# Optimization experiments

Measured on AMD Instinct MI355X. Metric: run time of the kernel, lower is better.

## Reference

```python
import jax, jax.numpy as jnp
import numpy as np

D_MODEL = 1024
NUM_HEADS = 16
HEAD_DIM = D_MODEL // NUM_HEADS
B, S = 4, 2048


def setup_inputs() -> dict:
    key = jax.random.key(0)
    ks = jax.random.split(key, 11)
    sc = 1.0 / np.sqrt(D_MODEL)
    return {
        "query": jax.random.normal(ks[0], (B, S, D_MODEL), jnp.float32),
        "key": jax.random.normal(ks[1], (B, S, D_MODEL), jnp.float32),
        "value": jax.random.normal(ks[2], (B, S, D_MODEL), jnp.float32),
        "Wq": jax.random.normal(ks[3], (D_MODEL, D_MODEL), jnp.float32) * sc,
        "bq": jnp.zeros((D_MODEL,), jnp.float32),
        "Wk": jax.random.normal(ks[4], (D_MODEL, D_MODEL), jnp.float32) * sc,
        "bk": jnp.zeros((D_MODEL,), jnp.float32),
        "Wv": jax.random.normal(ks[5], (D_MODEL, D_MODEL), jnp.float32) * sc,
        "bv": jnp.zeros((D_MODEL,), jnp.float32),
        "Wo": jax.random.normal(ks[6], (D_MODEL, D_MODEL), jnp.float32) * sc,
        "bo": jnp.zeros((D_MODEL,), jnp.float32),
    }


def _split_heads(x):
    b, s, _ = x.shape
    return x.reshape(b, s, NUM_HEADS, HEAD_DIM).transpose(0, 2, 1, 3)  # [B,H,S,Dh]


def reference(query, key, value, Wq, bq, Wk, bk, Wv, bv, Wo, bo):
    q = _split_heads(query @ Wq + bq)
    k = _split_heads(key @ Wk + bk)
    v = _split_heads(value @ Wv + bv)
    scores = jnp.einsum("bhqd,bhkd->bhqk", q, k) / np.sqrt(HEAD_DIM)
    attn = jax.nn.softmax(scores, axis=-1)
    out = jnp.einsum("bhqk,bhkd->bhqd", attn, v)
    out = out.transpose(0, 2, 1, 3).reshape(query.shape[0], -1, D_MODEL)
    return out @ Wo + bo
```

## Files before the change

kernel.cpp:

```cpp
#include <hip/hip_runtime.h>

typedef unsigned short u16;
typedef unsigned int   u32;
typedef unsigned long long u64;
typedef __attribute__((ext_vector_type(8))) short bf16x8;
typedef __attribute__((ext_vector_type(4))) float f32x4;

#define S_  2048
#define DH  64
#define DM  1024
#define BS  8192
#define CS  0.18033688011112042f

static __device__ __forceinline__ float bf2f(u16 v){ return __uint_as_float(((u32)v)<<16); }
static __device__ __forceinline__ u16 f2bf(float f){
  u32 x = __float_as_uint(f);
  return (u16)((x + 0x7fffu + ((x>>16)&1u)) >> 16);
}
#if __has_builtin(__builtin_amdgcn_cvt_pk_bf16_f32)
static __device__ __forceinline__ u32 pk2(float x, float y){
  typedef __attribute__((ext_vector_type(2))) __bf16 bf2v;
  union { bf2v v; u32 u; } c; c.v = __builtin_amdgcn_cvt_pk_bf16_f32(x, y); return c.u;
}
#else
static __device__ __forceinline__ u32 pk2(float x, float y){
  return (u32)f2bf(x) | ((u32)f2bf(y) << 16);
}
#endif
#if __has_builtin(__builtin_amdgcn_exp2f)
#define EXP2F(x) __builtin_amdgcn_exp2f(x)
#else
#define EXP2F(x) exp2f(x)
#endif

static __device__ __forceinline__ void dma16(const u16* g, const u16* l){
  __builtin_amdgcn_global_load_lds(
      (const __attribute__((address_space(1))) u32*)(u64)(uintptr_t)g,
      (__attribute__((address_space(3))) u32*)(u32)(u64)(uintptr_t)l, 16, 0, 0);
}

static __device__ __forceinline__ bf16x8 lds_frag(const u16* p){
  union { bf16x8 f; uint2 u[2]; } w;
  w.u[0] = *(const uint2*)(p);
  w.u[1] = *(const uint2*)(p+4);
  return w.f;
}
static __device__ __forceinline__ bf16x8 frag16v(const u16* p){
  union { bf16x8 f; uint4 u; } w;
  w.u = *(const uint4*)p;
  return w.f;
}
static __device__ __forceinline__ void stage16_bf(const u16* __restrict__ g, u16* s){
  uint4 a = *(const uint4*)g;
  uint4 b = *(const uint4*)(g+8);
  *(uint2*)(s+0)  = make_uint2(a.x,a.y);
  *(uint2*)(s+4)  = make_uint2(a.z,a.w);
  *(uint2*)(s+8)  = make_uint2(b.x,b.y);
  *(uint2*)(s+12) = make_uint2(b.z,b.w);
}
static __device__ __forceinline__ void stage16_f32(const float* __restrict__ g, u16* s){
  float4 a0 = ((const float4*)g)[0];
  float4 a1 = ((const float4*)g)[1];
  float4 a2 = ((const float4*)g)[2];
  float4 a3 = ((const float4*)g)[3];
  *(uint2*)(s+0)  = make_uint2(pk2(a0.x,a0.y), pk2(a0.z,a0.w));
  *(uint2*)(s+4)  = make_uint2(pk2(a1.x,a1.y), pk2(a1.z,a1.w));
  *(uint2*)(s+8)  = make_uint2(pk2(a2.x,a2.y), pk2(a2.z,a2.w));
  *(uint2*)(s+12) = make_uint2(pk2(a3.x,a3.y), pk2(a3.z,a3.w));
}

__global__ __launch_bounds__(256) void prep(
    const void* __restrict__ w0, const void* __restrict__ w1,
    const void* __restrict__ w2, const void* __restrict__ w3,
    u16* t0, u16* t1, u16* t2, u16* t3,
    const void* __restrict__ a0, const void* __restrict__ a1,
    const void* __restrict__ a2,
    u16* c0, u16* c1, u16* c2, const int f32f){
  __shared__ u16 tile[32][33];
  int z = blockIdx.z;
  int tid = threadIdx.x;
  bool f32 = f32f != 0;
  if (z < 4){
    const void* in = z==0?w0 : z==1?w1 : z==2?w2 : w3;
    u16* out = z==0?t0 : z==1?t1 : z==2?t2 : t3;
    int tx = tid & 31, ty = tid >> 5;
    int c  = blockIdx.x*32 + tx;
    int r0 = blockIdx.y*32;
    for (int i=ty;i<32;i+=8){
      long off = (long)(r0+i)*DM + c;
      tile[i][tx] = f32 ? f2bf(((const float*)in)[off]) : ((const u16*)in)[off];
    }
    __syncthreads();
    int rr = r0 + tx, cb = blockIdx.x*32;
    for (int i=ty;i<32;i+=8) out[(long)(cb+i)*DM + rr] = tile[tx][i];
  } else {
    if (!f32) return;
    const void* in = z==4?a0 : z==5?a1 : a2;
    u16* out = z==4?c0 : z==5?c1 : c2;
    long lb = (long)blockIdx.y*32 + blockIdx.x;
    long base = (lb*256 + tid)*8;
    #pragma unroll
    for (int it=0; it<4; it++){
      long i = base + (long)it*2097152;
      const float4* p = (const float4*)((const float*)in + i);
      float4 x = p[0], y = p[1];
      *(uint4*)(out + i) = make_uint4(pk2(x.x,x.y), pk2(x.z,x.w), pk2(y.x,y.y), pk2(y.z,y.w));
    }
  }
}

template<int ADMA>
__global__ __launch_bounds__(256) void gemm_qkv(
    const void* __restrict__ A0, const void* __restrict__ A1, const void* __restrict__ A2,
    const u16* __restrict__ W0, const u16* __restrict__ W1, const u16* __restrict__ W2,
    const void* __restrict__ bv0, const void* __restrict__ bv1, const void* __restrict__ bv2,
    u16* C0, u16* C1, u16* C2, const int f32f){
  constexpr int AST = ADMA ? 32 : 36;
  constexpr int NB  = ADMA ? 2 : 1;
  __shared__ __align__(16) u16 As[NB][128*AST];
  __shared__ __align__(16) u16 Bs[NB][128*32];
  int z = blockIdx.z;
  const void* A  = z==0?A0 : z==1?A1 : A2;
  const u16* BT  = z==0?W0 : z==1?W1 : W2;
  const void* bias = z==0?bv0 : z==1?bv1 : bv2;
  u16* C = z==0?C0 : z==1?C1 : C2;
  const bool aF32 = (!ADMA) && (f32f != 0);
  const bool bF32 = (f32f != 0);
  int tid = threadIdx.x;
  int by = blockIdx.x, bx = blockIdx.y;
  int lane = tid & 63, w = tid >> 6;
  int t = lane & 15, q = lane >> 4;
  int wr = w >> 1, wc = w & 1;
  f32x4 acc[4][4];
  #pragma unroll
  for(int i=0;i<4;i++) for(int j=0;j<4;j++) for(int k=0;k<4;k++) acc[i][j][k]=0.f;

  if constexpr (ADMA){
    int sl = (lane & 7) ^ (lane >> 3);
    int srow = ((lane >> 3) << 1) + (sl >> 2);
    const u16* gA = (const u16*)A + ((long)(by*128 + w*32 + srow)*DM + (sl&3)*8);
    const u16* gB = BT            + ((long)(bx*128 + w*32 + srow)*DM + (sl&3)*8);
    const int lb = w*1024;
    int rdo = ((t>>1)<<6) + (((((t&1)<<2) | q) ^ (t>>1)) << 3);
    dma16(gA,         &As[0][lb]);
    dma16(gA + 16*DM, &As[0][lb + 512]);
    dma16(gB,         &Bs[0][lb]);
    dma16(gB + 16*DM, &Bs[0][lb + 512]);
    for (int k0=0; k0<DM; k0+=32){
      int cur = (k0>>5)&1;
      if (k0+32 < DM){
        dma16(gA + k0+32,         &As[cur^1][lb]);
        dma16(gA + k0+32 + 16*DM, &As[cur^1][lb + 512]);
        dma16(gB + k0+32,         &Bs[cur^1][lb]);
        dma16(gB + k0+32 + 16*DM, &Bs[cur^1][lb + 512]);
        asm volatile("s_waitcnt vmcnt(4)" ::: "memory");
      } else {
        asm volatile("s_waitcnt vmcnt(0)" ::: "memory");
      }
      __builtin_amdgcn_s_barrier();
      bf16x8 af[4], bfr[4];
      const u16* Ar = &As[cur][wr*2048 + rdo];
      const u16* Br = &Bs[cur][wc*2048 + rdo];
      #pragma unroll
      for (int rt=0;rt<4;rt++) af[rt]  = frag16v(Ar + rt*512);
      #pragma unroll
      for (int ct=0;ct<4;ct++) bfr[ct] = frag16v(Br + ct*512);
      #pragma unroll
      for (int rt=0;rt<4;rt++)
        #pragma unroll
        for (int ct=0;ct<4;ct++)
          acc[rt][ct] = __builtin_amdgcn_mfma_f32_16x16x32_bf16(af[rt], bfr[ct], acc[rt][ct], 0,0,0);
      __builtin_amdgcn_s_barrier();
    }
  } else {
    const u16* gB = BT + ((long)(bx*128 + w*32 + (lane>>2))*DM + (lane&3)*8);
    long aoff = (long)(by*128 + (tid>>1))*DM + (tid&1)*16;
    const u16* ArdB = &As[0][(wr*64 + t)*AST + q*8];
    const u16* BrdB = &Bs[0][(wc*64 + t)*32  + q*8];
    for (int k0=0; k0<DM; k0+=32){
      dma16(gB + k0,         &Bs[0][w*1024]);
      dma16(gB + 16*DM + k0, &Bs[0][w*1024 + 512]);
      u16* AsW = &As[0][(tid>>1)*36 + (tid&1)*16];
      if (aF32) stage16_f32((const float*)A + aoff + k0, AsW);
      else      stage16_bf ((const u16*)A  + aoff + k0, AsW);
      __syncthreads();
      bf16x8 af[4], bfr[4];
      #pragma unroll
      for (int rt=0;rt<4;rt++) af[rt]  = lds_frag(ArdB + rt*16*AST);
      #pragma unroll
      for (int ct=0;ct<4;ct++) bfr[ct] = lds_frag(BrdB + ct*16*32);
      #pragma unroll
      for (int rt=0;rt<4;rt++)
        #pragma unroll
        for (int ct=0;ct<4;ct++)
          acc[rt][ct] = __builtin_amdgcn_mfma_f32_16x16x32_bf16(af[rt], bfr[ct], acc[rt][ct], 0,0,0);
      __syncthreads();
    }
  }

  float scale = (z==0) ? CS : 1.0f;
  #pragma unroll
  for (int ct=0;ct<4;ct++){
    int col = bx*128 + wc*64 + ct*16 + t;
    float bvv = bF32 ? ((const float*)bias)[col] : bf2f(((const u16*)bias)[col]);
    #pragma unroll
    for (int rt=0;rt<4;rt++){
      int row0 = by*128 + wr*64 + rt*16 + q*4;
      if (z == 2){
        int bb = row0 >> 11, s = row0 & 2047;
        long vbase = (long)bb*2097152 + (long)col*2048
                   + (s & ~63) + ((rt>>1)<<5) + (q<<3) + ((rt&1)<<2);
        u32 lo = pk2(acc[rt][ct][0]+bvv, acc[rt][ct][1]+bvv);
        u32 hi = pk2(acc[rt][ct][2]+bvv, acc[rt][ct][3]+bvv);
        *(uint2*)(C + vbase) = make_uint2(lo,hi);
      } else {
        #pragma unroll
        for (int r=0;r<4;r++)
          C[(long)(row0+r)*DM + col] = f2bf((acc[rt][ct][r] + bvv)*scale);
      }
    }
  }
}

__global__ __launch_bounds__(256) void gemm_o(const u16* __restrict__ A,
    const u16* __restrict__ BT, const void* __restrict__ bias, void* __restrict__ C,
    const int f32f){
  __shared__ __align__(16) u16 As[2][128*32];
  __shared__ __align__(16) u16 Bs[2][128*32];
  const int f = f32f;
  int tid = threadIdx.x;
  int by = blockIdx.x, bx = blockIdx.y;
  int lane = tid & 63, w = tid >> 6;
  int t = lane & 15, q = lane >> 4;
  int wr = w >> 1, wc = w & 1;
  f32x4 acc[4][4];
  #pragma unroll
  for(int i=0;i<4;i++) for(int j=0;j<4;j++) for(int k=0;k<4;k++) acc[i][j][k]=0.f;

  int sl = (lane & 7) ^ (lane >> 3);
  int srow = ((lane >> 3) << 1) + (sl >> 2);
  const u16* gA = A  + ((long)(by*128 + w*32 + srow)*DM + (sl&3)*8);
  const u16* gB = BT + ((long)(bx*128 + w*32 + srow)*DM + (sl&3)*8);
  const int lb = w*1024;
  int rdo = ((t>>1)<<6) + (((((t&1)<<2) | q) ^ (t>>1)) << 3);
  dma16(gA,         &As[0][lb]);
  dma16(gA + 16*DM, &As[0][lb + 512]);
  dma16(gB,         &Bs[0][lb]);
  dma16(gB + 16*DM, &Bs[0][lb + 512]);
  for (int k0=0; k0<DM; k0+=32){
    int cur = (k0>>5)&1;
    if (k0+32 < DM){
      dma16(gA + k0+32,         &As[cur^1][lb]);
      dma16(gA + k0+32 + 16*DM, &As[cur^1][lb + 512]);
      dma16(gB + k0+32,         &Bs[cur^1][lb]);
      dma16(gB + k0+32 + 16*DM, &Bs[cur^1][lb + 512]);
      asm volatile("s_waitcnt vmcnt(4)" ::: "memory");
    } else {
      asm volatile("s_waitcnt vmcnt(0)" ::: "memory");
    }
    __builtin_amdgcn_s_barrier();
    bf16x8 af[4], bfr[4];
    const u16* Ar = &As[cur][wr*2048 + rdo];
    const u16* Br = &Bs[cur][wc*2048 + rdo];
    #pragma unroll
    for (int rt=0;rt<4;rt++) af[rt]  = frag16v(Ar + rt*512);
    #pragma unroll
    for (int ct=0;ct<4;ct++) bfr[ct] = frag16v(Br + ct*512);
    #pragma unroll
    for (int rt=0;rt<4;rt++)
      #pragma unroll
      for (int ct=0;ct<4;ct++)
        acc[rt][ct] = __builtin_amdgcn_mfma_f32_16x16x32_bf16(af[rt], bfr[ct], acc[rt][ct], 0,0,0);
    __builtin_amdgcn_s_barrier();
  }
  #pragma unroll
  for (int ct=0;ct<4;ct++){
    int col = bx*128 + wc*64 + ct*16 + t;
    float bvv = f ? ((const float*)bias)[col] : bf2f(((const u16*)bias)[col]);
    #pragma unroll
    for (int rt=0;rt<4;rt++){
      int row0 = by*128 + wr*64 + rt*16 + q*4;
      #pragma unroll
      for (int r=0;r<4;r++){
        long idx = (long)(row0+r)*DM + col;
        float v = acc[rt][ct][r] + bvv;
        if (f) ((float*)C)[idx] = v;
        else   ((u16*)C)[idx]  = f2bf(v);
      }
    }
  }
}

__global__ __launch_bounds__(256,4) void attn5(const u16* __restrict__ Q,
    const u16* __restrict__ Kb, const u16* __restrict__ Vt, u16* __restrict__ O){
  __shared__ __align__(16) u16 Ks[2][4096];
  __shared__ __align__(16) u16 Vs[2][4096];
  int tid = threadIdx.x;
  int bid = blockIdx.x;
  int qt = bid >> 6;
  int s6 = bid & 63;
  int bh = (s6 & 7)*8 + (s6 >> 3);
  int b = bh >> 4, h = bh & 15;
  int lane = tid & 63, w = tid >> 6;
  int t = lane & 15, q = lane >> 4;

  const u16* Qbase = Q + ((long)(b*S_ + qt*128 + w*32 + t)*DM + h*DH + q*8);
  bf16x8 qf[2][2];
  qf[0][0] = frag16v(Qbase);
  qf[0][1] = frag16v(Qbase + 32);
  qf[1][0] = frag16v(Qbase + 16*DM);
  qf[1][1] = frag16v(Qbase + 16*DM + 32);

  int r0 = tid >> 3;
  int cb = ((tid & 7) * 16) ^ ((r0 & 7) << 4);
  const char* gK = (const char*)Kb + (((long)(b*S_ + r0)*DM + h*DH) << 1) + cb;
  const char* gV = (const char*)Vt + ((((long)bh << 17) + ((long)r0 << 11)) << 1) + cb;
  const long gK1 = ((long)32*DM) << 1;
  const long gV1 = ((long)32*S_) << 1;
  const int ld0 = w*512, ld1 = 2048 + w*512;

  f32x4 o[2][4];
  #pragma unroll
  for (int i=0;i<2;i++) for (int j=0;j<4;j++) for (int k=0;k<4;k++) o[i][j][k]=0.f;
  f32x4 o4[2];
  #pragma unroll
  for (int i=0;i<2;i++) for (int k=0;k<4;k++) o4[i][k]=0.f;

  const f32x4 z4 = {0.f, 0.f, 0.f, 0.f};

  union { bf16x8 f; u32 u[4]; } vone;
  { u32 ovv = (t==0) ? 0x3F803F80u : 0u;
    vone.u[0]=ovv; vone.u[1]=ovv; vone.u[2]=ovv; vone.u[3]=ovv; }

  const int xorv = (t & 7) << 4;

  dma16((const u16*)(gK),       &Ks[0][ld0]);
  dma16((const u16*)(gK + gK1), &Ks[0][ld1]);
  dma16((const u16*)(gV),       &Vs[0][ld0]);
  dma16((const u16*)(gV + gV1), &Vs[0][ld1]);

  for (int kt=0; kt<32; kt++){
    int cur = kt & 1;
    if (kt < 31){
      long ko = ((long)(kt+1)*64*DM) << 1;
      long vo = (long)(kt+1) << 7;
      dma16((const u16*)(gK + ko),       &Ks[cur^1][ld0]);
      dma16((const u16*)(gK + ko + gK1), &Ks[cur^1][ld1]);
      dma16((const u16*)(gV + vo),       &Vs[cur^1][ld0]);
      dma16((const u16*)(gV + vo + gV1), &Vs[cur^1][ld1]);
      asm volatile("s_waitcnt vmcnt(4)" ::: "memory");
    } else {
      asm volatile("s_waitcnt vmcnt(0)" ::: "memory");
    }
    __builtin_amdgcn_s_barrier();

    const u16* Kc = Ks[cur];
    const u16* Vc = Vs[cur];

    f32x4 sacc[2][4];
    {
      int off = ((q*16) ^ xorv) >> 1;
      bf16x8 k0 = frag16v(Kc + (t     )*64 + off);
      bf16x8 k1 = frag16v(Kc + (16 + t)*64 + off);
      bf16x8 k2 = frag16v(Kc + (32 + t)*64 + off);
      bf16x8 k3 = frag16v(Kc + (48 + t)*64 + off);
      __builtin_amdgcn_s_setprio(1);
      #pragma unroll
      for (int rt=0; rt<2; rt++){
        sacc[rt][0] = __builtin_amdgcn_mfma_f32_16x16x32_bf16(k0, qf[rt][0], z4, 0,0,0);
        sacc[rt][1] = __builtin_amdgcn_mfma_f32_16x16x32_bf16(k1, qf[rt][0], z4, 0,0,0);
        sacc[rt][2] = __builtin_amdgcn_mfma_f32_16x16x32_bf16(k2, qf[rt][0], z4, 0,0,0);
        sacc[rt][3] = __builtin_amdgcn_mfma_f32_16x16x32_bf16(k3, qf[rt][0], z4, 0,0,0);
      }
      __builtin_amdgcn_s_setprio(0);
    }
    {
      int off = ((64 + q*16) ^ xorv) >> 1;
      bf16x8 k0 = frag16v(Kc + (t     )*64 + off);
      bf16x8 k1 = frag16v(Kc + (16 + t)*64 + off);
      bf16x8 k2 = frag16v(Kc + (32 + t)*64 + off);
      bf16x8 k3 = frag16v(Kc + (48 + t)*64 + off);
      __builtin_amdgcn_s_setprio(1);
      #pragma unroll
      for (int rt=0; rt<2; rt++){
        sacc[rt][0] = __builtin_amdgcn_mfma_f32_16x16x32_bf16(k0, qf[rt][1], sacc[rt][0],0,0,0);
        sacc[rt][1] = __builtin_amdgcn_mfma_f32_16x16x32_bf16(k1, qf[rt][1], sacc[rt][1],0,0,0);
        sacc[rt][2] = __builtin_amdgcn_mfma_f32_16x16x32_bf16(k2, qf[rt][1], sacc[rt][2],0,0,0);
        sacc[rt][3] = __builtin_amdgcn_mfma_f32_16x16x32_bf16(k3, qf[rt][1], sacc[rt][3],0,0,0);
      }
      __builtin_amdgcn_s_setprio(0);
    }

    union { bf16x8 f; u32 u[4]; } af[2][2];
    #pragma unroll
    for (int rt=0; rt<2; rt++){
      float ev[4][4];
      #pragma unroll
      for (int c=0; c<4; c++)
        #pragma unroll
        for (int r=0; r<4; r++) ev[c][r] = EXP2F(sacc[rt][c][r]);
      #pragma unroll
      for (int ks=0; ks<2; ks++){
        af[rt][ks].u[0] = pk2(ev[2*ks  ][0], ev[2*ks  ][1]);
        af[rt][ks].u[1] = pk2(ev[2*ks  ][2], ev[2*ks  ][3]);
        af[rt][ks].u[2] = pk2(ev[2*ks+1][0], ev[2*ks+1][1]);
        af[rt][ks].u[3] = pk2(ev[2*ks+1][2], ev[2*ks+1][3]);
      }
    }

    #pragma unroll
    for (int ks=0; ks<2; ks++){
      int off = ((ks*64 + q*16) ^ xorv) >> 1;
      bf16x8 v0 = frag16v(Vc + (t     )*64 + off);
      bf16x8 v1 = frag16v(Vc + (16 + t)*64 + off);
      bf16x8 v2 = frag16v(Vc + (32 + t)*64 + off);
      bf16x8 v3 = frag16v(Vc + (48 + t)*64 + off);
      __builtin_amdgcn_s_setprio(1);
      #pragma unroll
      for (int rt=0; rt<2; rt++){
        o[rt][0] = __builtin_amdgcn_mfma_f32_16x16x32_bf16(af[rt][ks].f, v0, o[rt][0],0,0,0);
        o[rt][1] = __builtin_amdgcn_mfma_f32_16x16x32_bf16(af[rt][ks].f, v1, o[rt][1],0,0,0);
        o[rt][2] = __builtin_amdgcn_mfma_f32_16x16x32_bf16(af[rt][ks].f, v2, o[rt][2],0,0,0);
        o[rt][3] = __builtin_amdgcn_mfma_f32_16x16x32_bf16(af[rt][ks].f, v3, o[rt][3],0,0,0);
        o4[rt]   = __builtin_amdgcn_mfma_f32_16x16x32_bf16(af[rt][ks].f, vone.f, o4[rt],0,0,0);
      }
      __builtin_amdgcn_s_setprio(0);
    }
    __builtin_amdgcn_s_barrier();
  }

  #pragma unroll
  for (int rt=0; rt<2; rt++){
    #pragma unroll
    for (int r=0; r<4; r++){
      float l = __shfl(o4[rt][r], lane & 48);
      float inv = 1.f / l;
      int row = qt*128 + w*32 + rt*16 + q*4 + r;
      #pragma unroll
      for (int ct=0; ct<4; ct++)
        O[(long)(b*S_ + row)*DM + h*DH + ct*16 + t] = f2bf(o[rt][ct][r] * inv);
    }
  }
}

extern "C" void kernel_launch(void* const* d_in, const int* in_sizes, int n_in,
                              void* d_out, int out_size, void* d_ws, size_t ws_size,
                              hipStream_t stream){
  (void)n_in; (void)out_size;
  const void* xq = d_in[0];
  const void* xk = d_in[1];
  const void* xv = d_in[2];
  const void* Wq = d_in[3];
  const void* bq = d_in[4];
  const void* Wk = d_in[5];
  const void* bk = d_in[6];
  const void* Wv = d_in[7];
  const void* bv = d_in[8];
  const void* Wo = d_in[9];
  const void* bo = d_in[10];

  const long NT = (long)BS*DM;
  int f32f = 1;
  if (in_sizes && in_sizes[0] == (int)(NT*2)) f32f = 0;

  u16* base = (u16*)((char*)d_ws + 256);
  u16* Qb  = base;
  u16* Kbf = base + NT;
  u16* Vt  = base + 2*NT;
  u16* WqT = base + 3*NT;
  u16* WkT = WqT + (long)DM*DM;
  u16* WvT = WkT + (long)DM*DM;
  u16* WoT = WvT + (long)DM*DM;
  u16* Xc0 = WoT + (long)DM*DM;
  u16* Xc1 = Xc0 + NT;
  u16* Xc2 = Xc1 + NT;
  size_t need_pre = 256 + (size_t)(6*NT + 4*(long)DM*DM)*2;
  bool pre = ws_size >= need_pre;

  dim3 gb(256,1,1);
  int nz = (pre && f32f) ? 7 : 4;
  prep<<<dim3(32,32,nz), gb, 0, stream>>>(Wq, Wk, Wv, Wo,
      WqT, WkT, WvT, WoT, xq, xk, xv, Xc0, Xc1, Xc2, f32f);

  if (pre){
    const void* Aq = f32f ? (const void*)Xc0 : xq;
    const void* Ak = f32f ? (const void*)Xc1 : xk;
    const void* Av = f32f ? (const void*)Xc2 : xv;
    gemm_qkv<1><<<dim3(64,8,3), gb, 0, stream>>>(Aq, Ak, Av,
        WqT, WkT, WvT, bq, bk, bv, Qb, Kbf, Vt, f32f);
  } else {
    gemm_qkv<0><<<dim3(64,8,3), gb, 0, stream>>>(xq, xk, xv,
        WqT, WkT, WvT, bq, bk, bv, Qb, Kbf, Vt, f32f);
  }

  attn5<<<dim3(1024,1,1), gb, 0, stream>>>(Qb, Kbf, Vt, Qb );

  gemm_o<<<dim3(64,8,1), gb, 0, stream>>>(Qb, WoT, bo, d_out, f32f);
}
```

Baseline: 350.7 us.

## Enlarge GEMM tiles to 256x128x64 with 512 threads and XOR-swizzled LDS

```diff
diff --git a/kernel.cpp b/kernel.cpp
--- a/kernel.cpp
+++ b/kernel.cpp
@@ -39,34 +39,10 @@
       (__attribute__((address_space(3))) u32*)(u32)(u64)(uintptr_t)l, 16, 0, 0);
 }
 
-static __device__ __forceinline__ bf16x8 lds_frag(const u16* p){
-  union { bf16x8 f; uint2 u[2]; } w;
-  w.u[0] = *(const uint2*)(p);
-  w.u[1] = *(const uint2*)(p+4);
-  return w.f;
-}
 static __device__ __forceinline__ bf16x8 frag16v(const u16* p){
   union { bf16x8 f; uint4 u; } w;
   w.u = *(const uint4*)p;
   return w.f;
-}
-static __device__ __forceinline__ void stage16_bf(const u16* __restrict__ g, u16* s){
-  uint4 a = *(const uint4*)g;
-  uint4 b = *(const uint4*)(g+8);
-  *(uint2*)(s+0)  = make_uint2(a.x,a.y);
-  *(uint2*)(s+4)  = make_uint2(a.z,a.w);
-  *(uint2*)(s+8)  = make_uint2(b.x,b.y);
-  *(uint2*)(s+12) = make_uint2(b.z,b.w);
-}
-static __device__ __forceinline__ void stage16_f32(const float* __restrict__ g, u16* s){
-  float4 a0 = ((const float4*)g)[0];
-  float4 a1 = ((const float4*)g)[1];
-  float4 a2 = ((const float4*)g)[2];
-  float4 a3 = ((const float4*)g)[3];
-  *(uint2*)(s+0)  = make_uint2(pk2(a0.x,a0.y), pk2(a0.z,a0.w));
-  *(uint2*)(s+4)  = make_uint2(pk2(a1.x,a1.y), pk2(a1.z,a1.w));
-  *(uint2*)(s+8)  = make_uint2(pk2(a2.x,a2.y), pk2(a2.z,a2.w));
-  *(uint2*)(s+12) = make_uint2(pk2(a3.x,a3.y), pk2(a3.z,a3.w));
 }
 
 __global__ __launch_bounds__(256) void prep(
@@ -109,22 +85,19 @@
   }
 }
 
-template<int ADMA>
-__global__ __launch_bounds__(256) void gemm_qkv(
-    const void* __restrict__ A0, const void* __restrict__ A1, const void* __restrict__ A2,
+
+__global__ __launch_bounds__(512) void gemm_qkv(
+    const u16* __restrict__ A0, const u16* __restrict__ A1, const u16* __restrict__ A2,
     const u16* __restrict__ W0, const u16* __restrict__ W1, const u16* __restrict__ W2,
     const void* __restrict__ bv0, const void* __restrict__ bv1, const void* __restrict__ bv2,
     u16* C0, u16* C1, u16* C2, const int f32f){
-  constexpr int AST = ADMA ? 32 : 36;
-  constexpr int NB  = ADMA ? 2 : 1;
-  __shared__ __align__(16) u16 As[NB][128*AST];
-  __shared__ __align__(16) u16 Bs[NB][128*32];
+  __shared__ __align__(16) u16 As[2][256*64];
+  __shared__ __align__(16) u16 Bs[2][128*64];
   int z = blockIdx.z;
-  const void* A  = z==0?A0 : z==1?A1 : A2;
-  const u16* BT  = z==0?W0 : z==1?W1 : W2;
+  const u16* A  = z==0?A0 : z==1?A1 : A2;
+  const u16* BT = z==0?W0 : z==1?W1 : W2;
   const void* bias = z==0?bv0 : z==1?bv1 : bv2;
   u16* C = z==0?C0 : z==1?C1 : C2;
-  const bool aF32 = (!ADMA) && (f32f != 0);
   const bool bF32 = (f32f != 0);
   int tid = threadIdx.x;
   int by = blockIdx.x, bx = blockIdx.y;
@@ -135,66 +108,47 @@
   #pragma unroll
   for(int i=0;i<4;i++) for(int j=0;j<4;j++) for(int k=0;k<4;k++) acc[i][j][k]=0.f;
 
-  if constexpr (ADMA){
-    int sl = (lane & 7) ^ (lane >> 3);
-    int srow = ((lane >> 3) << 1) + (sl >> 2);
-    const u16* gA = (const u16*)A + ((long)(by*128 + w*32 + srow)*DM + (sl&3)*8);
-    const u16* gB = BT            + ((long)(bx*128 + w*32 + srow)*DM + (sl&3)*8);
-    const int lb = w*1024;
-    int rdo = ((t>>1)<<6) + (((((t&1)<<2) | q) ^ (t>>1)) << 3);
-    dma16(gA,         &As[0][lb]);
-    dma16(gA + 16*DM, &As[0][lb + 512]);
-    dma16(gB,         &Bs[0][lb]);
-    dma16(gB + 16*DM, &Bs[0][lb + 512]);
-    for (int k0=0; k0<DM; k0+=32){
-      int cur = (k0>>5)&1;
-      if (k0+32 < DM){
-        dma16(gA + k0+32,         &As[cur^1][lb]);
-        dma16(gA + k0+32 + 16*DM, &As[cur^1][lb + 512]);
-        dma16(gB + k0+32,         &Bs[cur^1][lb]);
-        dma16(gB + k0+32 + 16*DM, &Bs[cur^1][lb + 512]);
-        asm volatile("s_waitcnt vmcnt(4)" ::: "memory");
-      } else {
-        asm volatile("s_waitcnt vmcnt(0)" ::: "memory");
-      }
-      __builtin_amdgcn_s_barrier();
+  int sl = (lane & 7) ^ (lane >> 3);
+  const u16* gA = A  + ((long)(by*256 + w*8 + (lane>>3))*DM + sl*8);
+  const u16* gB = BT + ((long)(bx*128 + w*8 + (lane>>3))*DM + sl*8);
+
+  #pragma unroll
+  for (int i=0;i<4;i++) dma16(gA + (long)i*64*DM,      &As[0][(i*64 + w*8)*64]);
+  #pragma unroll
+  for (int j=0;j<2;j++) dma16(gB + (long)j*64*DM,      &Bs[0][(j*64 + w*8)*64]);
+  #pragma unroll
+  for (int i=0;i<4;i++) dma16(gA + (long)i*64*DM + 64, &As[1][(i*64 + w*8)*64]);
+  #pragma unroll
+  for (int j=0;j<2;j++) dma16(gB + (long)j*64*DM + 64, &Bs[1][(j*64 + w*8)*64]);
+
+  for (int kt=0; kt<16; kt++){
+    int buf = kt & 1;
+    if (kt < 15) asm volatile("s_waitcnt vmcnt(6)" ::: "memory");
+    else         asm volatile("s_waitcnt vmcnt(0)" ::: "memory");
+    __builtin_amdgcn_s_barrier();
+    #pragma unroll
+    for (int kk=0; kk<2; kk++){
       bf16x8 af[4], bfr[4];
-      const u16* Ar = &As[cur][wr*2048 + rdo];
-      const u16* Br = &Bs[cur][wc*2048 + rdo];
-      #pragma unroll
-      for (int rt=0;rt<4;rt++) af[rt]  = frag16v(Ar + rt*512);
-      #pragma unroll
-      for (int ct=0;ct<4;ct++) bfr[ct] = frag16v(Br + ct*512);
+      int so = (((kk*4 + q) ^ (t&7)) << 3);
+      #pragma unroll
+      for (int rt=0;rt<4;rt++) af[rt]  = frag16v(&As[buf][(wr*64 + rt*16 + t)*64 + so]);
+      #pragma unroll
+      for (int ct=0;ct<4;ct++) bfr[ct] = frag16v(&Bs[buf][(wc*64 + ct*16 + t)*64 + so]);
+      __builtin_amdgcn_s_setprio(1);
       #pragma unroll
       for (int rt=0;rt<4;rt++)
         #pragma unroll
         for (int ct=0;ct<4;ct++)
           acc[rt][ct] = __builtin_amdgcn_mfma_f32_16x16x32_bf16(af[rt], bfr[ct], acc[rt][ct], 0,0,0);
-      __builtin_amdgcn_s_barrier();
-    }
-  } else {
-    const u16* gB = BT + ((long)(bx*128 + w*32 + (lane>>2))*DM + (lane&3)*8);
-    long aoff = (long)(by*128 + (tid>>1))*DM + (tid&1)*16;
-    const u16* ArdB = &As[0][(wr*64 + t)*AST + q*8];
-    const u16* BrdB = &Bs[0][(wc*64 + t)*32  + q*8];
-    for (int k0=0; k0<DM; k0+=32){
-      dma16(gB + k0,         &Bs[0][w*1024]);
-      dma16(gB + 16*DM + k0, &Bs[0][w*1024 + 512]);
-      u16* AsW = &As[0][(tid>>1)*36 + (tid&1)*16];
-      if (aF32) stage16_f32((const float*)A + aoff + k0, AsW);
-      else      stage16_bf ((const u16*)A  + aoff + k0, AsW);
-      __syncthreads();
-      bf16x8 af[4], bfr[4];
-      #pragma unroll
-      for (int rt=0;rt<4;rt++) af[rt]  = lds_frag(ArdB + rt*16*AST);
-      #pragma unroll
-      for (int ct=0;ct<4;ct++) bfr[ct] = lds_frag(BrdB + ct*16*32);
-      #pragma unroll
-      for (int rt=0;rt<4;rt++)
-        #pragma unroll
-        for (int ct=0;ct<4;ct++)
-          acc[rt][ct] = __builtin_amdgcn_mfma_f32_16x16x32_bf16(af[rt], bfr[ct], acc[rt][ct], 0,0,0);
-      __syncthreads();
+      __builtin_amdgcn_s_setprio(0);
+    }
+    __builtin_amdgcn_s_barrier();
+    if (kt + 2 < 16){
+      int k0 = (kt+2)*64;
+      #pragma unroll
+      for (int i=0;i<4;i++) dma16(gA + (long)i*64*DM + k0, &As[buf][(i*64 + w*8)*64]);
+      #pragma unroll
+      for (int j=0;j<2;j++) dma16(gB + (long)j*64*DM + k0, &Bs[buf][(j*64 + w*8)*64]);
     }
   }
 
@@ -205,7 +159,7 @@
     float bvv = bF32 ? ((const float*)bias)[col] : bf2f(((const u16*)bias)[col]);
     #pragma unroll
     for (int rt=0;rt<4;rt++){
-      int row0 = by*128 + wr*64 + rt*16 + q*4;
+      int row0 = by*256 + wr*64 + rt*16 + q*4;
       if (z == 2){
         int bb = row0 >> 11, s = row0 & 2047;
         long vbase = (long)bb*2097152 + (long)col*2048
@@ -222,11 +176,11 @@
   }
 }
 
-__global__ __launch_bounds__(256) void gemm_o(const u16* __restrict__ A,
+__global__ __launch_bounds__(512) void gemm_o(const u16* __restrict__ A,
     const u16* __restrict__ BT, const void* __restrict__ bias, void* __restrict__ C,
     const int f32f){
-  __shared__ __align__(16) u16 As[2][128*32];
-  __shared__ __align__(16) u16 Bs[2][128*32];
+  __shared__ __align__(16) u16 As[2][256*64];
+  __shared__ __align__(16) u16 Bs[2][128*64];
   const int f = f32f;
   int tid = threadIdx.x;
   int by = blockIdx.x, bx = blockIdx.y;
@@ -238,48 +192,56 @@
   for(int i=0;i<4;i++) for(int j=0;j<4;j++) for(int k=0;k<4;k++) acc[i][j][k]=0.f;
 
   int sl = (lane & 7) ^ (lane >> 3);
-  int srow = ((lane >> 3) << 1) + (sl >> 2);
-  const u16* gA = A  + ((long)(by*128 + w*32 + srow)*DM + (sl&3)*8);
-  const u16* gB = BT + ((long)(bx*128 + w*32 + srow)*DM + (sl&3)*8);
-  const int lb = w*1024;
-  int rdo = ((t>>1)<<6) + (((((t&1)<<2) | q) ^ (t>>1)) << 3);
-  dma16(gA,         &As[0][lb]);
-  dma16(gA + 16*DM, &As[0][lb + 512]);
-  dma16(gB,         &Bs[0][lb]);
-  dma16(gB + 16*DM, &Bs[0][lb + 512]);
-  for (int k0=0; k0<DM; k0+=32){
-    int cur = (k0>>5)&1;
-    if (k0+32 < DM){
-      dma16(gA + k0+32,         &As[cur^1][lb]);
-      dma16(gA + k0+32 + 16*DM, &As[cur^1][lb + 512]);
-      dma16(gB + k0+32,         &Bs[cur^1][lb]);
-      dma16(gB + k0+32 + 16*DM, &Bs[cur^1][lb + 512]);
-      asm volatile("s_waitcnt vmcnt(4)" ::: "memory");
-    } else {
-      asm volatile("s_waitcnt vmcnt(0)" ::: "memory");
-    }
-    __builtin_amdgcn_s_barrier();
-    bf16x8 af[4], bfr[4];
-    const u16* Ar = &As[cur][wr*2048 + rdo];
-    const u16* Br = &Bs[cur][wc*2048 + rdo];
-    #pragma unroll
-    for (int rt=0;rt<4;rt++) af[rt]  = frag16v(Ar + rt*512);
-    #pragma unroll
-    for (int ct=0;ct<4;ct++) bfr[ct] = frag16v(Br + ct*512);
-    #pragma unroll
-    for (int rt=0;rt<4;rt++)
-      #pragma unroll
-      for (int ct=0;ct<4;ct++)
-        acc[rt][ct] = __builtin_amdgcn_mfma_f32_16x16x32_bf16(af[rt], bfr[ct], acc[rt][ct], 0,0,0);
-    __builtin_amdgcn_s_barrier();
-  }
+  const u16* gA = A  + ((long)(by*256 + w*8 + (lane>>3))*DM + sl*8);
+  const u16* gB = BT + ((long)(bx*128 + w*8 + (lane>>3))*DM + sl*8);
+
+  #pragma unroll
+  for (int i=0;i<4;i++) dma16(gA + (long)i*64*DM,      &As[0][(i*64 + w*8)*64]);
+  #pragma unroll
+  for (int j=0;j<2;j++) dma16(gB + (long)j*64*DM,      &Bs[0][(j*64 + w*8)*64]);
+  #pragma unroll
+  for (int i=0;i<4;i++) dma16(gA + (long)i*64*DM + 64, &As[1][(i*64 + w*8)*64]);
+  #pragma unroll
+  for (int j=0;j<2;j++) dma16(gB + (long)j*64*DM + 64, &Bs[1][(j*64 + w*8)*64]);
+
+  for (int kt=0; kt<16; kt++){
+    int buf = kt & 1;
+    if (kt < 15) asm volatile("s_waitcnt vmcnt(6)" ::: "memory");
+    else         asm volatile("s_waitcnt vmcnt(0)" ::: "memory");
+    __builtin_amdgcn_s_barrier();
+    #pragma unroll
+    for (int kk=0; kk<2; kk++){
+      bf16x8 af[4], bfr[4];
+      int so = (((kk*4 + q) ^ (t&7)) << 3);
+      #pragma unroll
+      for (int rt=0;rt<4;rt++) af[rt]  = frag16v(&As[buf][(wr*64 + rt*16 + t)*64 + so]);
+      #pragma unroll
+      for (int ct=0;ct<4;ct++) bfr[ct] = frag16v(&Bs[buf][(wc*64 + ct*16 + t)*64 + so]);
+      __builtin_amdgcn_s_setprio(1);
+      #pragma unroll
+      for (int rt=0;rt<4;rt++)
+        #pragma unroll
+        for (int ct=0;ct<4;ct++)
+          acc[rt][ct] = __builtin_amdgcn_mfma_f32_16x16x32_bf16(af[rt], bfr[ct], acc[rt][ct], 0,0,0);
+      __builtin_amdgcn_s_setprio(0);
+    }
+    __builtin_amdgcn_s_barrier();
+    if (kt + 2 < 16){
+      int k0 = (kt+2)*64;
+      #pragma unroll
+      for (int i=0;i<4;i++) dma16(gA + (long)i*64*DM + k0, &As[buf][(i*64 + w*8)*64]);
+      #pragma unroll
+      for (int j=0;j<2;j++) dma16(gB + (long)j*64*DM + k0, &Bs[buf][(j*64 + w*8)*64]);
+    }
+  }
+
   #pragma unroll
   for (int ct=0;ct<4;ct++){
     int col = bx*128 + wc*64 + ct*16 + t;
     float bvv = f ? ((const float*)bias)[col] : bf2f(((const u16*)bias)[col]);
     #pragma unroll
     for (int rt=0;rt<4;rt++){
-      int row0 = by*128 + wr*64 + rt*16 + q*4;
+      int row0 = by*256 + wr*64 + rt*16 + q*4;
       #pragma unroll
       for (int r=0;r<4;r++){
         long idx = (long)(row0+r)*DM + col;
@@ -446,7 +408,7 @@
 extern "C" void kernel_launch(void* const* d_in, const int* in_sizes, int n_in,
                               void* d_out, int out_size, void* d_ws, size_t ws_size,
                               hipStream_t stream){
-  (void)n_in; (void)out_size;
+  (void)n_in; (void)out_size; (void)ws_size;
   const void* xq = d_in[0];
   const void* xk = d_in[1];
   const void* xv = d_in[2];
@@ -474,26 +436,19 @@
   u16* Xc0 = WoT + (long)DM*DM;
   u16* Xc1 = Xc0 + NT;
   u16* Xc2 = Xc1 + NT;
-  size_t need_pre = 256 + (size_t)(6*NT + 4*(long)DM*DM)*2;
-  bool pre = ws_size >= need_pre;
 
   dim3 gb(256,1,1);
-  int nz = (pre && f32f) ? 7 : 4;
+  int nz = f32f ? 7 : 4;
   prep<<<dim3(32,32,nz), gb, 0, stream>>>(Wq, Wk, Wv, Wo,
       WqT, WkT, WvT, WoT, xq, xk, xv, Xc0, Xc1, Xc2, f32f);
 
-  if (pre){
-    const void* Aq = f32f ? (const void*)Xc0 : xq;
-    const void* Ak = f32f ? (const void*)Xc1 : xk;
-    const void* Av = f32f ? (const void*)Xc2 : xv;
-    gemm_qkv<1><<<dim3(64,8,3), gb, 0, stream>>>(Aq, Ak, Av,
-        WqT, WkT, WvT, bq, bk, bv, Qb, Kbf, Vt, f32f);
-  } else {
-    gemm_qkv<0><<<dim3(64,8,3), gb, 0, stream>>>(xq, xk, xv,
-        WqT, WkT, WvT, bq, bk, bv, Qb, Kbf, Vt, f32f);
-  }
+  const u16* Aq = f32f ? Xc0 : (const u16*)xq;
+  const u16* Ak = f32f ? Xc1 : (const u16*)xk;
+  const u16* Av = f32f ? Xc2 : (const u16*)xv;
+  gemm_qkv<<<dim3(32,8,3), dim3(512,1,1), 0, stream>>>(Aq, Ak, Av,
+      WqT, WkT, WvT, bq, bk, bv, Qb, Kbf, Vt, f32f);
 
   attn5<<<dim3(1024,1,1), gb, 0, stream>>>(Qb, Kbf, Vt, Qb );
 
-  gemm_o<<<dim3(64,8,1), gb, 0, stream>>>(Qb, WoT, bo, d_out, f32f);
-}
+  gemm_o<<<dim3(32,8,1), dim3(512,1,1), 0, stream>>>(Qb, WoT, bo, d_out, f32f);
+}
```

Measured after the change: 343.3 us. -2.1%, faster.
